# Kernel tuning notes

Hardware: AMD Instinct MI355X
Metric: run time of the kernel (lower is better)

Reference implementation:

```python
import jax, jax.numpy as jnp
import numpy as np

O, T = 2000, 6000
DIN, DW, DG, H = 2048, 300, 512, 512
VO, VR, L_EXTRA = 1000, 500, 4


def _mlp2(x, Wa, ba, Wb, bb):
    # two-layer MLP with ReLU after every Linear (sg2im build_mlp, final_nonlinearity=True)
    return jax.nn.relu(jax.nn.relu(x @ Wa + ba) @ Wb + bb)


def _triple_conv(obj_vecs, pred_vecs, s, o, Wa, ba, Wb, bb, W2a, b2a, W2b, b2b, alpha=1.0):
    # gather-by-edge -> edge MLP -> scatter-avg back to nodes (GraphTripleConv, pooling='avg')
    n_obj = obj_vecs.shape[0]
    dout = W2b.shape[1]
    cur = jnp.concatenate([obj_vecs[s], pred_vecs, obj_vecs[o]], axis=1)  # [T, 2*Din+Dp]
    t = _mlp2(cur, Wa, ba, Wb, bb)                                        # [T, 2H+Dout]
    new_s, new_p, new_o = t[:, :H], t[:, H:H + dout], t[:, H + dout:]
    pooled = jnp.zeros((n_obj, H), t.dtype).at[s].add(new_s).at[o].add(new_o)
    cnt = jnp.zeros((n_obj,), t.dtype).at[s].add(1.0).at[o].add(1.0)
    pooled = pooled / jnp.maximum(cnt, 1.0)[:, None]
    new_obj = alpha * _mlp2(pooled, W2a, b2a, W2b, b2b)
    return new_obj, new_p


def setup_inputs() -> dict:
    key = jax.random.key(0)
    ks = jax.random.split(key, 32)
    w = lambda k, sh: (jax.random.normal(k, sh, jnp.float32) * 0.02)
    inp = {
        'obj_embs': jax.random.normal(ks[0], (O, DIN), jnp.float32),
        'obj_nums': O,
        'pred_embs': jax.random.normal(ks[1], (T, DIN), jnp.float32),
        'pred_nums': T,
        'rels': jax.random.randint(ks[2], (T, 3), 0, VR, jnp.int64 if jax.config.read('jax_enable_x64') else jnp.int32),
        'objs': jax.random.randint(ks[3], (O,), 0, VO, jnp.int64 if jax.config.read('jax_enable_x64') else jnp.int32),
        # embedding tables
        'obj_table': jax.random.uniform(ks[4], (VO, DW), jnp.float32, -0.1, 0.1),
        'rel_table': jax.random.uniform(ks[5], (VR, DW), jnp.float32, -0.1, 0.1),
        # fusion layers: Linear(img_dim+word_dim -> img_dim) + relu
        'Wf_obj': w(ks[6], (DIN + DW, DIN)), 'bf_obj': jnp.zeros((DIN,), jnp.float32),
        'Wf_rel': w(ks[7], (DIN + DW, DIN)), 'bf_rel': jnp.zeros((DIN,), jnp.float32),
        # GraphTripleConv layer 1: net1 [3*DIN -> H -> 2H+DG], net2 [H -> H -> DG]
        'W1a': w(ks[8], (3 * DIN, H)), 'b1a': jnp.zeros((H,), jnp.float32),
        'W1b': w(ks[9], (H, 2 * H + DG)), 'b1b': jnp.zeros((2 * H + DG,), jnp.float32),
        'W2a': w(ks[10], (H, H)), 'b2a': jnp.zeros((H,), jnp.float32),
        'W2b': w(ks[11], (H, DG)), 'b2b': jnp.zeros((DG,), jnp.float32),
        # GraphTripleConvNet: 4 more layers, net1 [3*DG -> H -> 2H+DG], net2 [H -> H -> DG]
        'Ws1a': w(ks[12], (L_EXTRA, 3 * DG, H)), 'bs1a': jnp.zeros((L_EXTRA, H), jnp.float32),
        'Ws1b': w(ks[13], (L_EXTRA, H, 2 * H + DG)), 'bs1b': jnp.zeros((L_EXTRA, 2 * H + DG), jnp.float32),
        'Ws2a': w(ks[14], (L_EXTRA, H, H)), 'bs2a': jnp.zeros((L_EXTRA, H), jnp.float32),
        'Ws2b': w(ks[15], (L_EXTRA, H, DG)), 'bs2b': jnp.zeros((L_EXTRA, DG), jnp.float32),
    }
    return inp


def reference(obj_embs, obj_nums, pred_embs, pred_nums, rels, objs,
              obj_table, rel_table, Wf_obj, bf_obj, Wf_rel, bf_rel,
              W1a, b1a, W1b, b1b, W2a, b2a, W2b, b2b,
              Ws1a, bs1a, Ws1b, bs1b, Ws2a, bs2a, Ws2b, bs2b):
    s, p, o = rels[:, 0], rels[:, 1], rels[:, 2]
    # embedding lookup + concatenate-fusion (FusionLayer with relu)
    obj_vecs = jax.nn.relu(jnp.concatenate([obj_embs, obj_table[objs]], axis=1) @ Wf_obj + bf_obj)
    pred_vecs = jax.nn.relu(jnp.concatenate([pred_embs, rel_table[p]], axis=1) @ Wf_rel + bf_rel)
    # first GraphTripleConv (img_dim -> gconv_dim)
    obj_vecs, pred_vecs = _triple_conv(obj_vecs, pred_vecs, s, o,
                                       W1a, b1a, W1b, b1b, W2a, b2a, W2b, b2b)
    # GraphTripleConvNet: 4 more layers (gconv_dim -> gconv_dim)
    for i in range(L_EXTRA):
        obj_vecs, pred_vecs = _triple_conv(obj_vecs, pred_vecs, s, o,
                                           Ws1a[i], bs1a[i], Ws1b[i], bs1b[i],
                                           Ws2a[i], bs2a[i], Ws2b[i], bs2b[i])
    # no_imgnorm=True -> no final l2norm
    return obj_vecs, pred_vecs
```

## Files before the change

### kernel.cpp

```cpp
#include <hip/hip_runtime.h>

#define O_N 2000
#define T_N 6000
#define DIN 2048
#define DW  300
#define DG  512
#define HH_ 512

typedef __attribute__((ext_vector_type(8)))  short short8;
typedef __attribute__((ext_vector_type(16))) float f32x16;
typedef unsigned short u16;

__device__ __forceinline__ float4 ld4(const float* p) { return *(const float4*)p; }

__device__ __forceinline__ u16 rbf(float x) {
    unsigned int u = __float_as_uint(x);
    u += 0x7FFFu + ((u >> 16) & 1u);
    return (u16)(u >> 16);
}
__device__ __forceinline__ float fbf(u16 h) {
    return __uint_as_float((unsigned int)h << 16);
}
__device__ __forceinline__ void split3(float x, short& h, short& m, short& l) {
    u16 a = rbf(x);
    float r = x - fbf(a);
    u16 b = rbf(r);
    r -= fbf(b);
    u16 c = rbf(r);
    h = (short)a; m = (short)b; l = (short)c;
}

__device__ __forceinline__ void gl_lds16(u16* lds, const u16* g) {
    auto* gp = (const __attribute__((address_space(1))) unsigned int*)g;
    auto* lp = (__attribute__((address_space(3))) unsigned int*)lds;
    __builtin_amdgcn_global_load_lds(gp, lp, 16, 0, 0);
}

template<int BM, int BN, int KS>
__global__ __launch_bounds__(KS ? 512 : 256, KS ? 2 : (BM == 64 ? 4 : 2))
void gemm_mx(
    const u16* __restrict__ Ap, int MpA,
    const u16* __restrict__ Bp, int N, int KC, int M,
    const float* __restrict__ bias, int doRelu,
    float* __restrict__ C, int ldc,
    u16* __restrict__ Op, int MpO,
    const u16* __restrict__ Bp2, float* __restrict__ C2, u16* __restrict__ Op2,
    int nbx)
{
    static_assert(BM == 128 || BM == 64, "BM in {64,128}");
    constexpr int WM = BM / 2, WN = BN / 2;
    constexpr int FI = WM / 32, FJ = WN / 32;
    static_assert(!KS || FI == 2, "KS path needs FI=2");
    constexpr int UA = 6 * BM;
    constexpr int UB = 6 * BN;
    constexpr int NI = (UA + UB) / 64;
    constexpr int II = (NI + 3) / 4;
    constexpr int LDMIN = NI / 4;
    constexpr int BUF = (BM + BN) * 48;
    __shared__ u16 sm[(KS ? 6 : 3) * BUF];

    const int tid = threadIdx.x;
    const int w = tid >> 6, lane = tid & 63;
    const int wg = w & 3;
    const int g = KS ? (w >> 2) : 0;
    const int ln31 = lane & 31, lq = lane >> 5;

    int bx = blockIdx.x;
    const u16* Bpl = Bp; float* Cl = C; u16* Opl = Op;
    if (bx >= nbx) { bx -= nbx; Bpl = Bp2; Cl = C2; Opl = Op2; }
    const int n0 = bx * BN, m0 = blockIdx.y * BM;
    const long psA = (long)KC * MpA * 8;
    const long psB = (long)KC * N * 8;

    int c0 = 0, cn = KC;
    if (KS) { int h = (KC >> 2) << 1; c0 = g ? h : 0; cn = g ? (KC - h) : h; }
    const u16* ApG = Ap + (long)c0 * MpA * 8;
    const u16* BpG = Bpl + (long)c0 * N * 8;
    u16* smg = sm + g * 3 * BUF;

    const u16* gb[II]; int gstep[II]; int lob[II]; bool gv[II];
#pragma unroll
    for (int ii = 0; ii < II; ii++) {
        int n = wg + 4 * ii;
        gv[ii] = n < NI;
        int nn = gv[ii] ? n : 0;
        int u0 = nn * 64;
        bool isA = u0 < UA;
        int uu = isA ? u0 : u0 - UA;
        int dim = isA ? BM : BN;
        int row0 = uu % dim, pq = uu / dim;
        int q = pq & 1, p = pq >> 1;
        const u16* pb = (isA ? ApG : BpG) + (long)p * (isA ? psA : psB);
        int mp = isA ? MpA : N;
        gb[ii] = pb + ((long)q * mp + (isA ? m0 : n0) + row0 + lane) * 8;
        gstep[ii] = mp * 16;
        lob[ii] = (isA ? (pq * BM + row0) : (6 * BM + pq * BN + row0)) * 8;
    }

    f32x16 ah[FI][FJ], al[FI][FJ];
#pragma unroll
    for (int fi = 0; fi < FI; fi++)
#pragma unroll
        for (int fj = 0; fj < FJ; fj++)
#pragma unroll
            for (int r = 0; r < 16; r++) { ah[fi][fj][r] = 0.f; al[fi][fj][r] = 0.f; }

    const int T = cn >> 1;
#pragma unroll
    for (int ii = 0; ii < II; ii++)
        if (gv[ii]) gl_lds16(smg + lob[ii], gb[ii]);
    if (T > 1) {
#pragma unroll
        for (int ii = 0; ii < II; ii++)
            if (gv[ii]) gl_lds16(smg + BUF + lob[ii], gb[ii] + (long)gstep[ii]);
    }
#pragma unroll
    for (int ii = 0; ii < II; ii++) gb[ii] += (long)2 * gstep[ii];

    int cb = 0, sb = 2 * BUF;
    for (int t = 0; t < T; t++) {
        if (t + 1 < T) asm volatile("s_waitcnt vmcnt(%0)" :: "i"(LDMIN) : "memory");
        else           asm volatile("s_waitcnt vmcnt(0)" ::: "memory");
        __builtin_amdgcn_s_barrier();
        asm volatile("" ::: "memory");

        if (t + 2 < T) {
#pragma unroll
            for (int ii = 0; ii < II; ii++)
                if (gv[ii]) { gl_lds16(smg + sb + lob[ii], gb[ii]); gb[ii] += (long)gstep[ii]; }
        }

        const u16* ab = smg + cb;
        const u16* bb = ab + 6 * BM * 8;
        short8 af[FI][3], bf[FJ][3];
#pragma unroll
        for (int fi = 0; fi < FI; fi++)
#pragma unroll
            for (int p = 0; p < 3; p++)
                af[fi][p] = *(const short8*)(ab + ((p * 2 + lq) * BM + (wg >> 1) * WM + fi * 32 + ln31) * 8);
#pragma unroll
        for (int fj = 0; fj < FJ; fj++) {
            const int rB = (wg & 1) * WN + fj * 32 + ln31;
#pragma unroll
            for (int p = 0; p < 3; p++)
                bf[fj][p] = *(const short8*)(bb + ((p * 2 + lq) * BN + rB) * 8);
        }

#pragma unroll
        for (int fj = 0; fj < FJ; fj++) {
#pragma unroll
            for (int fi = 0; fi < FI; fi++) {
                ah[fi][fj] = __builtin_amdgcn_mfma_f32_32x32x16_bf16(af[fi][0], bf[fj][0], ah[fi][fj], 0, 0, 0);
                al[fi][fj] = __builtin_amdgcn_mfma_f32_32x32x16_bf16(af[fi][0], bf[fj][1], al[fi][fj], 0, 0, 0);
                al[fi][fj] = __builtin_amdgcn_mfma_f32_32x32x16_bf16(af[fi][1], bf[fj][0], al[fi][fj], 0, 0, 0);
                al[fi][fj] = __builtin_amdgcn_mfma_f32_32x32x16_bf16(af[fi][0], bf[fj][2], al[fi][fj], 0, 0, 0);
                al[fi][fj] = __builtin_amdgcn_mfma_f32_32x32x16_bf16(af[fi][1], bf[fj][1], al[fi][fj], 0, 0, 0);
                al[fi][fj] = __builtin_amdgcn_mfma_f32_32x32x16_bf16(af[fi][2], bf[fj][0], al[fi][fj], 0, 0, 0);
            }
        }

        cb += BUF; if (cb == 3 * BUF) cb = 0;
        sb += BUF; if (sb == 3 * BUF) sb = 0;
    }
    __syncthreads();

    float tv[FJ][16];
    if (KS) {
        constexpr int XW = FJ * 16 * 64;
        float* xs = (float*)sm;
        float* wrp = xs + (1 - g) * 4 * XW + wg * XW;
        if (g == 0) {
#pragma unroll
            for (int fj = 0; fj < FJ; fj++)
#pragma unroll
                for (int r = 0; r < 16; r++)
                    wrp[(fj * 16 + r) * 64 + lane] = ah[1][fj][r] + al[1][fj][r];
        } else {
#pragma unroll
            for (int fj = 0; fj < FJ; fj++)
#pragma unroll
                for (int r = 0; r < 16; r++)
                    wrp[(fj * 16 + r) * 64 + lane] = ah[0][fj][r] + al[0][fj][r];
        }
        __syncthreads();
        float* rdp = xs + g * 4 * XW + wg * XW;
        if (g == 0) {
#pragma unroll
            for (int fj = 0; fj < FJ; fj++)
#pragma unroll
                for (int r = 0; r < 16; r++)
                    tv[fj][r] = ah[0][fj][r] + al[0][fj][r] + rdp[(fj * 16 + r) * 64 + lane];
        } else {
#pragma unroll
            for (int fj = 0; fj < FJ; fj++)
#pragma unroll
                for (int r = 0; r < 16; r++)
                    tv[fj][r] = ah[1][fj][r] + al[1][fj][r] + rdp[(fj * 16 + r) * 64 + lane];
        }
        __syncthreads();
    }

    float* bounce = (float*)sm + w * 1184;
    const long psO = (long)N * MpO;
#pragma unroll
    for (int fi = 0; fi < FI; fi++) {
        if (KS && fi != g) continue;
#pragma unroll
        for (int fj = 0; fj < FJ; fj++) {
            const int colBase = n0 + (wg & 1) * WN + fj * 32;
            const int rowBase = m0 + (wg >> 1) * WM + fi * 32;
            float bv = bias ? bias[colBase + ln31] : 0.f;
            float v[16];
#pragma unroll
            for (int r = 0; r < 16; r++) {
                float s = KS ? tv[fj][r] : (ah[fi][fj][r] + al[fi][fj][r]);
                float x = s + bv;
                if (doRelu) x = fmaxf(x, 0.f);
                v[r] = x;
            }
            if (Cl) {
#pragma unroll
                for (int r = 0; r < 16; r++) {
                    int row = rowBase + (r & 3) + 8 * (r >> 2) + 4 * lq;
                    if (row < M)
                        Cl[(long)row * ldc + colBase + ln31] = v[r];
                }
            }
            if (Opl) {
#pragma unroll
                for (int r = 0; r < 16; r++)
                    bounce[((r & 3) + 8 * (r >> 2) + 4 * lq) * 36 + ln31] = v[r];
#pragma unroll
                for (int u = 0; u < 2; u++) {
                    int urow = ln31, uc = lq + 2 * u;
                    const float* rp = bounce + urow * 36 + uc * 8;
                    short8 h8, m8, l8;
#pragma unroll
                    for (int j = 0; j < 8; j++) {
                        short a, b, c2; split3(rp[j], a, b, c2);
                        h8[j] = a; m8[j] = b; l8[j] = c2;
                    }
                    long cIdx = (long)((colBase + uc * 8) >> 3);
                    long base = (cIdx * MpO + rowBase + urow) * 8;
                    *(short8*)(Opl + base) = h8;
                    *(short8*)(Opl + psO + base) = m8;
                    *(short8*)(Opl + 2 * psO + base) = l8;
                }
            }
        }
    }
}

__global__ __launch_bounds__(256) void split_b(
    const float* __restrict__ W, int K, int N, int KC,
    u16* __restrict__ Op)
{
    __shared__ float tl[64][65];
    const int tid = threadIdx.x;
    const int n0 = blockIdx.x * 64, k0 = blockIdx.y * 64;
    const long ps = (long)KC * N * 8;
#pragma unroll
    for (int l = 0; l < 4; l++) {
        int k = (tid >> 4) + l * 16;
        int nn = (tid & 15) << 2;
        float4 v = make_float4(0.f, 0.f, 0.f, 0.f);
        if (k0 + k < K) v = ld4(W + (long)(k0 + k) * N + n0 + nn);
        tl[k][nn] = v.x; tl[k][nn + 1] = v.y; tl[k][nn + 2] = v.z; tl[k][nn + 3] = v.w;
    }
    __syncthreads();
#pragma unroll
    for (int l = 0; l < 2; l++) {
        int u = tid + l * 256;
        int n = u & 63, c = u >> 6;
        short8 h8, m8, l8;
#pragma unroll
        for (int j = 0; j < 8; j++) {
            short a, b, c2; split3(tl[c * 8 + j][n], a, b, c2);
            h8[j] = a; m8[j] = b; l8[j] = c2;
        }
        long base = ((long)(k0 / 8 + c) * N + n0 + n) * 8;
        *(short8*)(Op + base) = h8;
        *(short8*)(Op + ps + base) = m8;
        *(short8*)(Op + 2 * ps + base) = l8;
    }
}

__device__ __forceinline__ void store_planes(u16* Op, long ps, long base, const float* x)
{
    short8 h8, m8, l8;
#pragma unroll
    for (int j = 0; j < 8; j++) {
        short a, b, c2; split3(x[j], a, b, c2);
        h8[j] = a; m8[j] = b; l8[j] = c2;
    }
    *(short8*)(Op + base) = h8;
    *(short8*)(Op + ps + base) = m8;
    *(short8*)(Op + 2 * ps + base) = l8;
}

__global__ __launch_bounds__(256) void split_concat_a(
    const float* __restrict__ E, int ldE, int KA,
    const float* __restrict__ Tab, int DWc,
    const int* __restrict__ idx, int idxStride,
    int mBase, int Mvalid, int Mp, int KC,
    u16* __restrict__ Op)
{
    int m = blockIdx.x * 256 + threadIdx.x;
    if (m >= Mp) return;
    int c = blockIdx.y;
    int gm = mBase + m;
    float x[8];
    if (gm >= Mvalid) {
#pragma unroll
        for (int j = 0; j < 8; j++) x[j] = 0.f;
    } else {
        int k0 = c * 8;
        if (k0 + 8 <= KA) {
            float4 a = ld4(E + (long)gm * ldE + k0);
            float4 b = ld4(E + (long)gm * ldE + k0 + 4);
            x[0] = a.x; x[1] = a.y; x[2] = a.z; x[3] = a.w;
            x[4] = b.x; x[5] = b.y; x[6] = b.z; x[7] = b.w;
        } else {
            const float* tr = Tab + (long)idx[(long)gm * idxStride] * DWc;
#pragma unroll
            for (int j = 0; j < 8; j++) {
                int k = k0 + j;
                x[j] = (k < KA) ? E[(long)gm * ldE + k]
                                : ((k - KA) < DWc ? tr[k - KA] : 0.f);
            }
        }
    }
    store_planes(Op, (long)KC * Mp * 8, ((long)c * Mp + m) * 8, x);
}

__global__ __launch_bounds__(256) void edge_planes(
    const float* __restrict__ PPv, const float* __restrict__ P1v,
    const float* __restrict__ P2v, const int* __restrict__ rels,
    const float* __restrict__ b1a, int Mp, u16* __restrict__ Op)
{
    int m = blockIdx.x * 256 + threadIdx.x;
    if (m >= Mp) return;
    int c = blockIdx.y;
    float x[8];
    if (m >= T_N) {
#pragma unroll
        for (int j = 0; j < 8; j++) x[j] = 0.f;
    } else {
        int s = rels[3 * m], o = rels[3 * m + 2];
        const float* pp = PPv + (long)m * HH_ + c * 8;
        const float* p1 = P1v + (long)s * HH_ + c * 8;
        const float* p2 = P2v + (long)o * HH_ + c * 8;
        const float* bb = b1a + c * 8;
#pragma unroll
        for (int j = 0; j < 8; j++)
            x[j] = fmaxf(pp[j] + p1[j] + p2[j] + bb[j], 0.f);
    }
    store_planes(Op, (long)64 * Mp * 8, ((long)c * Mp + m) * 8, x);
}

__global__ __launch_bounds__(256) void pool_planes(
    const float* __restrict__ PO, const int* __restrict__ CNT,
    int Mp, u16* __restrict__ Op)
{
    int m = blockIdx.x * 256 + threadIdx.x;
    if (m >= Mp) return;
    int c = blockIdx.y;
    float x[8];
    if (m >= O_N) {
#pragma unroll
        for (int j = 0; j < 8; j++) x[j] = 0.f;
    } else {
        int cc = CNT[m]; float cf = 1.f / (float)(cc < 1 ? 1 : cc);
#pragma unroll
        for (int j = 0; j < 8; j++) x[j] = PO[(long)m * HH_ + c * 8 + j] * cf;
    }
    store_planes(Op, (long)64 * Mp * 8, ((long)c * Mp + m) * 8, x);
}

__global__ __launch_bounds__(256) void predcopy_planes(
    const float* __restrict__ T2, int Mp, u16* __restrict__ Op)
{
    int m = blockIdx.x * 256 + threadIdx.x;
    if (m >= Mp) return;
    int c = blockIdx.y;
    float x[8];
    if (m >= T_N) {
#pragma unroll
        for (int j = 0; j < 8; j++) x[j] = 0.f;
    } else {
#pragma unroll
        for (int j = 0; j < 8; j++) x[j] = T2[(long)m * 1536 + 512 + c * 8 + j];
    }
    store_planes(Op, (long)64 * Mp * 8, ((long)c * Mp + m) * 8, x);
}

__global__ void predcopy_f32(const float* __restrict__ T2, float* __restrict__ dst)
{
    int i = blockIdx.x * 256 + threadIdx.x;
    if (i >= T_N * HH_ / 4) return;
    int e = i / (HH_ / 4);
    int j = (i % (HH_ / 4)) << 2;
    float4 v = ld4(T2 + (long)e * 1536 + 512 + j);
    *(float4*)(dst + (long)e * HH_ + j) = v;
}

__global__ void count_edges(const int* __restrict__ rels, int* __restrict__ CNT)
{
    int e = blockIdx.x * 256 + threadIdx.x;
    if (e >= T_N) return;
    atomicAdd(CNT + rels[3 * e + 0], 1);
    atomicAdd(CNT + rels[3 * e + 2], 1);
}

__global__ void scatter_pool(const float* __restrict__ T2,
                             const int* __restrict__ rels,
                             float* __restrict__ PO)
{
    int e = blockIdx.x;
    int t = threadIdx.x;
    int s = rels[e * 3 + 0];
    int o = rels[e * 3 + 2];
#pragma unroll
    for (int u = 0; u < 2; u++) {
        int j = t + u * 256;
        unsafeAtomicAdd(PO + (long)s * HH_ + j, T2[(long)e * 1536 + j]);
        unsafeAtomicAdd(PO + (long)o * HH_ + j, T2[(long)e * 1536 + 1024 + j]);
    }
}

template<int BM, int BN>
static inline void GX(hipStream_t st, const u16* Ap, int MpA,
                      const u16* Bp, int N, int KC, int M,
                      const float* bias, int relu_,
                      float* C, int ldc, u16* Op, int MpO,
                      const u16* Bp2, float* C2, u16* Op2)
{
    int nbx = N / BN;
    int pair = (Bp2 != nullptr) ? 2 : 1;
    dim3 g(nbx * pair, MpA / BM), b(256);
    gemm_mx<BM, BN, 0><<<g, b, 0, st>>>(Ap, MpA, Bp, N, KC, M, bias, relu_,
                                        C, ldc, Op, MpO, Bp2, C2, Op2, nbx);
}

template<int BM, int BN>
static inline void GK2(hipStream_t st, const u16* Ap, int MpA,
                       const u16* Bp, int N, int KC, int M,
                       const float* bias, int relu_,
                       float* C, int ldc, u16* Op, int MpO)
{
    dim3 g(N / BN, MpA / BM), b(512);
    gemm_mx<BM, BN, 1><<<g, b, 0, st>>>(Ap, MpA, Bp, N, KC, M, bias, relu_,
                                        C, ldc, Op, MpO,
                                        nullptr, nullptr, nullptr, N / BN);
}

static inline void SB(hipStream_t st, const float* W, int K, int N, int KC, u16* Op)
{
    dim3 g(N / 64, KC / 8), b(256);
    split_b<<<g, b, 0, st>>>(W, K, N, KC, Op);
}

extern "C" void kernel_launch(void* const* d_in, const int* in_sizes, int n_in,
                              void* d_out, int out_size, void* d_ws, size_t ws_size,
                              hipStream_t stream)
{
    const float* obj_embs  = (const float*)d_in[0];
    const float* pred_embs = (const float*)d_in[2];
    const int*   rels      = (const int*)d_in[4];
    const int*   objs      = (const int*)d_in[5];
    const float* obj_table = (const float*)d_in[6];
    const float* rel_table = (const float*)d_in[7];
    const float* Wf_obj = (const float*)d_in[8];
    const float* bf_obj = (const float*)d_in[9];
    const float* Wf_rel = (const float*)d_in[10];
    const float* bf_rel = (const float*)d_in[11];
    const float* W1a = (const float*)d_in[12];
    const float* b1a = (const float*)d_in[13];
    const float* W1b = (const float*)d_in[14];
    const float* b1b = (const float*)d_in[15];
    const float* W2a = (const float*)d_in[16];
    const float* b2a = (const float*)d_in[17];
    const float* W2b = (const float*)d_in[18];
    const float* b2b = (const float*)d_in[19];
    const float* Ws1a = (const float*)d_in[20];
    const float* bs1a = (const float*)d_in[21];
    const float* Ws1b = (const float*)d_in[22];
    const float* bs1b = (const float*)d_in[23];
    const float* Ws2a = (const float*)d_in[24];
    const float* bs2a = (const float*)d_in[25];
    const float* Ws2b = (const float*)d_in[26];
    const float* bs2b = (const float*)d_in[27];
    float* out = (float*)d_out;

    unsigned char* B8 = (unsigned char*)d_ws;
    constexpr size_t S1O  = 0;
    constexpr size_t S2O  = 29097984;
    constexpr size_t S3AO = 54263808;
    constexpr size_t ZSZ  = 86507520;
    constexpr size_t T2O  = 0;
    constexpr size_t TTO  = 36864000;
    constexpr size_t PVO  = 55345152;
    constexpr size_t PLO  = 73826304;
    constexpr size_t OVO  = 80117760;
    constexpr size_t S3BO = ZSZ;
    constexpr size_t S3CO = S3BO + 6291456;
    constexpr size_t PPO  = S3CO + 6291456;
    constexpr size_t P1O  = PPO + 12288000;
    constexpr size_t P2O  = P1O + 4096000;
    constexpr size_t CNO  = P2O + 4096000;

    u16* S1  = (u16*)(B8 + S1O);
    u16* S2  = (u16*)(B8 + S2O);
    u16* S3A = (u16*)(B8 + S3AO);
    u16* S3B = (u16*)(B8 + S3BO);
    u16* S3C = (u16*)(B8 + S3CO);
    float* T2 = (float*)(B8 + T2O);
    u16* TTp  = (u16*)(B8 + TTO);
    u16* Hp   = (u16*)(B8 + TTO);
    u16* PVp  = (u16*)(B8 + PVO);
    u16* PLp  = (u16*)(B8 + PLO);
    u16* OVp  = (u16*)(B8 + OVO);
    float* PP = (float*)(B8 + PPO);
    float* P1 = (float*)(B8 + P1O);
    float* P2 = (float*)(B8 + P2O);
    float* PO = P1;
    int* CNT  = (int*)(B8 + CNO);

    hipMemsetAsync(CNT, 0, O_N * sizeof(int), stream);
    hipLaunchKernelGGL(count_edges, dim3((T_N + 255) / 256), dim3(256), 0, stream, rels, CNT);

    SB(stream, Wf_obj, DIN + DW, DIN, 296, S3A);
    {
        dim3 g(8, 296), b(256);
        split_concat_a<<<g, b, 0, stream>>>(obj_embs, DIN, DIN, obj_table, DW,
                                            objs, 1, 0, O_N, 2048, 296, S1);
    }
    GK2<128, 128>(stream, S1, 2048, S3A, DIN, 296, O_N, bf_obj, 1,
                  nullptr, 0, S2, 2048);
    SB(stream, W1a, DIN, HH_, 256, S3B);
    SB(stream, W1a + (size_t)2 * DIN * HH_, DIN, HH_, 256, S3C);
    GX<64, 64>(stream, S2, 2048, S3B, HH_, 256, O_N, nullptr, 0,
               P1, HH_, nullptr, 0, S3C, P2, nullptr);
    SB(stream, Wf_rel, DIN + DW, DIN, 296, S3A);
    SB(stream, W1a + (size_t)DIN * HH_, DIN, HH_, 256, S3B);
    for (int ch = 0; ch < 3; ch++) {
        int ch0 = ch * 2048;
        int mp  = (ch == 2) ? 1920 : 2048;
        int mv  = (ch == 2) ? 1904 : 2048;
        dim3 g((mp + 255) / 256, 296), b(256);
        split_concat_a<<<g, b, 0, stream>>>(pred_embs, DIN, DIN, rel_table, DW,
                                            rels + 1, 3, ch0, T_N, mp, 296, S1);
        GK2<128, 128>(stream, S1, mp, S3A, DIN, 296, mv, bf_rel, 1,
                      nullptr, 0, S2, mp);
        GX<64, 64>(stream, S2, mp, S3B, HH_, 256, mv, nullptr, 0,
                   PP + (size_t)ch0 * HH_, HH_, nullptr, 0,
                   nullptr, nullptr, nullptr);
    }

    for (int L = 0; L < 5; L++) {
        const float* bb1a = (L == 0) ? b1a : (bs1a + (size_t)(L - 1) * HH_);
        const float* w1b  = (L == 0) ? W1b : (Ws1b + (size_t)(L - 1) * HH_ * 1536);
        const float* bb1b = (L == 0) ? b1b : (bs1b + (size_t)(L - 1) * 1536);
        const float* w2a  = (L == 0) ? W2a : (Ws2a + (size_t)(L - 1) * HH_ * HH_);
        const float* bb2a = (L == 0) ? b2a : (bs2a + (size_t)(L - 1) * HH_);
        const float* w2b  = (L == 0) ? W2b : (Ws2b + (size_t)(L - 1) * HH_ * DG);
        const float* bb2b = (L == 0) ? b2b : (bs2b + (size_t)(L - 1) * DG);

        if (L > 0) {
            const float* w1a = Ws1a + (size_t)(L - 1) * 3 * HH_ * HH_;
            SB(stream, w1a, HH_, HH_, 64, S3B);
            SB(stream, w1a + (size_t)2 * HH_ * HH_, HH_, HH_, 64, S3C);
            GX<64, 64>(stream, OVp, 2048, S3B, HH_, 64, O_N, nullptr, 0,
                       P1, HH_, nullptr, 0, S3C, P2, nullptr);
            SB(stream, w1a + (size_t)HH_ * HH_, HH_, HH_, 64, S3B);
            GX<64, 64>(stream, PVp, 6016, S3B, HH_, 64, T_N, nullptr, 0,
                       PP, HH_, nullptr, 0, nullptr, nullptr, nullptr);
        }

        {
            dim3 g(24, 64), b(256);
            edge_planes<<<g, b, 0, stream>>>(PP, P1, P2, rels, bb1a, 6016, TTp);
        }
        SB(stream, w1b, HH_, 1536, 64, S3C);
        GX<128, 128>(stream, TTp, 6016, S3C, 1536, 64, T_N, bb1b, 1,
                     T2, 1536, nullptr, 0, nullptr, nullptr, nullptr);
        hipMemsetAsync(PO, 0, (size_t)O_N * HH_ * sizeof(float), stream);
        hipLaunchKernelGGL(scatter_pool, dim3(T_N), dim3(256), 0, stream, T2, rels, PO);
        {
            dim3 g(8, 64), b(256);
            pool_planes<<<g, b, 0, stream>>>(PO, CNT, 2048, PLp);
        }
        SB(stream, w2a, HH_, HH_, 64, S3B);
        GX<64, 64>(stream, PLp, 2048, S3B, HH_, 64, O_N, bb2a, 1,
                   nullptr, 0, Hp, 2048, nullptr, nullptr, nullptr);
        SB(stream, w2b, HH_, DG, 64, S3C);
        if (L < 4) {
            GX<64, 64>(stream, Hp, 2048, S3C, DG, 64, O_N, bb2b, 1,
                       nullptr, 0, OVp, 2048, nullptr, nullptr, nullptr);
            dim3 g(24, 64), b(256);
            predcopy_planes<<<g, b, 0, stream>>>(T2, 6016, PVp);
        } else {
            GX<64, 64>(stream, Hp, 2048, S3C, DG, 64, O_N, bb2b, 1,
                       out, DG, nullptr, 0, nullptr, nullptr, nullptr);
            hipLaunchKernelGGL(predcopy_f32, dim3((T_N * HH_ / 4 + 255) / 256),
                               dim3(256), 0, stream, T2, out + (size_t)O_N * DG);
        }
    }
}
```

Before: 1.781 ms.

## Interleave LDS fragment loads with MFMA quadrants in split-K GEMM path

For the split-K (KS) GEMM variant, the main loop is restructured into four quadrant phases. Each phase loads the next A/B fragments from LDS and issues part of the global-to-LDS prefetch while the previous quadrant's MFMAs run. Barriers and s_setprio around each MFMA cluster keep the waves in step and favour matrix issue, and the next tile's first fragments are prefetched into registers. The non-KS path is unchanged. The cost is many more barriers per K step and extra register pressure from the double-buffered fragments.

```diff
diff --git a/kernel.cpp b/kernel.cpp
--- a/kernel.cpp
+++ b/kernel.cpp
@@ -35,6 +35,14 @@
     auto* lp = (__attribute__((address_space(3))) unsigned int*)lds;
     __builtin_amdgcn_global_load_lds(gp, lp, 16, 0, 0);
 }
+
+#define MFMA_Q(AX, BX, AH, AL) \
+    AH = __builtin_amdgcn_mfma_f32_32x32x16_bf16(AX[0], BX[0], AH, 0, 0, 0); \
+    AL = __builtin_amdgcn_mfma_f32_32x32x16_bf16(AX[0], BX[1], AL, 0, 0, 0); \
+    AL = __builtin_amdgcn_mfma_f32_32x32x16_bf16(AX[1], BX[0], AL, 0, 0, 0); \
+    AL = __builtin_amdgcn_mfma_f32_32x32x16_bf16(AX[0], BX[2], AL, 0, 0, 0); \
+    AL = __builtin_amdgcn_mfma_f32_32x32x16_bf16(AX[1], BX[1], AL, 0, 0, 0); \
+    AL = __builtin_amdgcn_mfma_f32_32x32x16_bf16(AX[2], BX[0], AL, 0, 0, 0);
 
 template<int BM, int BN, int KS>
 __global__ __launch_bounds__(KS ? 512 : 256, KS ? 2 : (BM == 64 ? 4 : 2))
@@ -50,7 +58,7 @@
     static_assert(BM == 128 || BM == 64, "BM in {64,128}");
     constexpr int WM = BM / 2, WN = BN / 2;
     constexpr int FI = WM / 32, FJ = WN / 32;
-    static_assert(!KS || FI == 2, "KS path needs FI=2");
+    static_assert(!KS || (FI == 2 && FJ == 2), "KS path needs 2x2 quadrants");
     constexpr int UA = 6 * BM;
     constexpr int UB = 6 * BN;
     constexpr int NI = (UA + UB) / 64;
@@ -106,61 +114,165 @@
             for (int r = 0; r < 16; r++) { ah[fi][fj][r] = 0.f; al[fi][fj][r] = 0.f; }
 
     const int T = cn >> 1;
-#pragma unroll
-    for (int ii = 0; ii < II; ii++)
-        if (gv[ii]) gl_lds16(smg + lob[ii], gb[ii]);
-    if (T > 1) {
+
+    if constexpr (KS) {
+#pragma unroll
+        for (int ii = 0; ii < II; ii++)
+            if (gv[ii]) gl_lds16(smg + lob[ii], gb[ii]);
 #pragma unroll
         for (int ii = 0; ii < II; ii++)
             if (gv[ii]) gl_lds16(smg + BUF + lob[ii], gb[ii] + (long)gstep[ii]);
-    }
-#pragma unroll
-    for (int ii = 0; ii < II; ii++) gb[ii] += (long)2 * gstep[ii];
-
-    int cb = 0, sb = 2 * BUF;
-    for (int t = 0; t < T; t++) {
-        if (t + 1 < T) asm volatile("s_waitcnt vmcnt(%0)" :: "i"(LDMIN) : "memory");
-        else           asm volatile("s_waitcnt vmcnt(0)" ::: "memory");
+#pragma unroll
+        for (int ii = 0; ii < II; ii++) gb[ii] += (long)2 * gstep[ii];
+
+        asm volatile("s_waitcnt vmcnt(%0)" :: "i"(II) : "memory");
         __builtin_amdgcn_s_barrier();
-        asm volatile("" ::: "memory");
-
-        if (t + 2 < T) {
+
+        const int rA = (wg >> 1) * WM + ln31;
+        const int rB = (wg & 1) * WN + ln31;
+        short8 A0[3], A1[3], B0[3], B1[3], A0n[3], B0n[3];
+        {
+            const u16* ab = smg;
+            const u16* bb = ab + 6 * BM * 8;
+#pragma unroll
+            for (int p = 0; p < 3; p++) {
+                A0[p] = *(const short8*)(ab + ((p * 2 + lq) * BM + rA) * 8);
+                B0[p] = *(const short8*)(bb + ((p * 2 + lq) * BN + rB) * 8);
+            }
+        }
+
+        int cb = 0, nb = BUF, sb = 2 * BUF;
+        for (int t = 0; t < T; t++) {
+            const u16* ab  = smg + cb;
+            const u16* bb  = ab + 6 * BM * 8;
+            const u16* abn = smg + nb;
+            const u16* bbn = abn + 6 * BM * 8;
+            const bool stg = (t + 2) < T;
+            const bool nxt = (t + 1) < T;
+
+#pragma unroll
+            for (int p = 0; p < 3; p++)
+                A1[p] = *(const short8*)(ab + ((p * 2 + lq) * BM + rA + 32) * 8);
+            if (stg) {
+#pragma unroll
+                for (int ii = 0; ii < 3; ii++)
+                    if (gv[ii]) gl_lds16(smg + sb + lob[ii], gb[ii]);
+            }
+            __builtin_amdgcn_s_barrier();
+            asm volatile("s_waitcnt lgkmcnt(0)" ::: "memory");
+            __builtin_amdgcn_s_setprio(1);
+            MFMA_Q(A0, B0, ah[0][0], al[0][0]);
+            __builtin_amdgcn_s_setprio(0);
+            __builtin_amdgcn_s_barrier();
+
+#pragma unroll
+            for (int p = 0; p < 3; p++)
+                B1[p] = *(const short8*)(bb + ((p * 2 + lq) * BN + rB + 32) * 8);
+            if (stg) {
+#pragma unroll
+                for (int ii = 3; ii < II; ii++)
+                    if (gv[ii]) gl_lds16(smg + sb + lob[ii], gb[ii]);
+            }
+            __builtin_amdgcn_s_barrier();
+            asm volatile("s_waitcnt lgkmcnt(0)" ::: "memory");
+            __builtin_amdgcn_s_setprio(1);
+            MFMA_Q(A1, B0, ah[1][0], al[1][0]);
+            __builtin_amdgcn_s_setprio(0);
+            __builtin_amdgcn_s_barrier();
+
+            if (nxt) {
+                if (stg) asm volatile("s_waitcnt vmcnt(%0)" :: "i"(II) : "memory");
+                else     asm volatile("s_waitcnt vmcnt(0)" ::: "memory");
+#pragma unroll
+                for (int p = 0; p < 3; p++)
+                    A0n[p] = *(const short8*)(abn + ((p * 2 + lq) * BM + rA) * 8);
+            }
+            __builtin_amdgcn_s_barrier();
+            asm volatile("s_waitcnt lgkmcnt(0)" ::: "memory");
+            __builtin_amdgcn_s_setprio(1);
+            MFMA_Q(A0, B1, ah[0][1], al[0][1]);
+            __builtin_amdgcn_s_setprio(0);
+            __builtin_amdgcn_s_barrier();
+
+            if (nxt) {
+#pragma unroll
+                for (int p = 0; p < 3; p++)
+                    B0n[p] = *(const short8*)(bbn + ((p * 2 + lq) * BN + rB) * 8);
+            }
+            __builtin_amdgcn_s_barrier();
+            asm volatile("s_waitcnt lgkmcnt(0)" ::: "memory");
+            __builtin_amdgcn_s_setprio(1);
+            MFMA_Q(A1, B1, ah[1][1], al[1][1]);
+            __builtin_amdgcn_s_setprio(0);
+            __builtin_amdgcn_s_barrier();
+
+            if (nxt) {
+#pragma unroll
+                for (int p = 0; p < 3; p++) { A0[p] = A0n[p]; B0[p] = B0n[p]; }
+            }
+            if (stg) {
+#pragma unroll
+                for (int ii = 0; ii < II; ii++) gb[ii] += (long)gstep[ii];
+            }
+            int tmp = cb; cb = nb; nb = sb; sb = tmp;
+        }
+    } else {
+#pragma unroll
+        for (int ii = 0; ii < II; ii++)
+            if (gv[ii]) gl_lds16(smg + lob[ii], gb[ii]);
+        if (T > 1) {
 #pragma unroll
             for (int ii = 0; ii < II; ii++)
-                if (gv[ii]) { gl_lds16(smg + sb + lob[ii], gb[ii]); gb[ii] += (long)gstep[ii]; }
-        }
-
-        const u16* ab = smg + cb;
-        const u16* bb = ab + 6 * BM * 8;
-        short8 af[FI][3], bf[FJ][3];
-#pragma unroll
-        for (int fi = 0; fi < FI; fi++)
-#pragma unroll
-            for (int p = 0; p < 3; p++)
-                af[fi][p] = *(const short8*)(ab + ((p * 2 + lq) * BM + (wg >> 1) * WM + fi * 32 + ln31) * 8);
-#pragma unroll
-        for (int fj = 0; fj < FJ; fj++) {
-            const int rB = (wg & 1) * WN + fj * 32 + ln31;
-#pragma unroll
-            for (int p = 0; p < 3; p++)
-                bf[fj][p] = *(const short8*)(bb + ((p * 2 + lq) * BN + rB) * 8);
-        }
-
-#pragma unroll
-        for (int fj = 0; fj < FJ; fj++) {
-#pragma unroll
-            for (int fi = 0; fi < FI; fi++) {
-                ah[fi][fj] = __builtin_amdgcn_mfma_f32_32x32x16_bf16(af[fi][0], bf[fj][0], ah[fi][fj], 0, 0, 0);
-                al[fi][fj] = __builtin_amdgcn_mfma_f32_32x32x16_bf16(af[fi][0], bf[fj][1], al[fi][fj], 0, 0, 0);
-                al[fi][fj] = __builtin_amdgcn_mfma_f32_32x32x16_bf16(af[fi][1], bf[fj][0], al[fi][fj], 0, 0, 0);
-                al[fi][fj] = __builtin_amdgcn_mfma_f32_32x32x16_bf16(af[fi][0], bf[fj][2], al[fi][fj], 0, 0, 0);
-                al[fi][fj] = __builtin_amdgcn_mfma_f32_32x32x16_bf16(af[fi][1], bf[fj][1], al[fi][fj], 0, 0, 0);
-                al[fi][fj] = __builtin_amdgcn_mfma_f32_32x32x16_bf16(af[fi][2], bf[fj][0], al[fi][fj], 0, 0, 0);
-            }
-        }
-
-        cb += BUF; if (cb == 3 * BUF) cb = 0;
-        sb += BUF; if (sb == 3 * BUF) sb = 0;
+                if (gv[ii]) gl_lds16(smg + BUF + lob[ii], gb[ii] + (long)gstep[ii]);
+        }
+#pragma unroll
+        for (int ii = 0; ii < II; ii++) gb[ii] += (long)2 * gstep[ii];
+
+        int cb = 0, sb = 2 * BUF;
+        for (int t = 0; t < T; t++) {
+            if (t + 1 < T) asm volatile("s_waitcnt vmcnt(%0)" :: "i"(LDMIN) : "memory");
+            else           asm volatile("s_waitcnt vmcnt(0)" ::: "memory");
+            __builtin_amdgcn_s_barrier();
+            asm volatile("" ::: "memory");
+
+            if (t + 2 < T) {
+#pragma unroll
+                for (int ii = 0; ii < II; ii++)
+                    if (gv[ii]) { gl_lds16(smg + sb + lob[ii], gb[ii]); gb[ii] += (long)gstep[ii]; }
+            }
+
+            const u16* ab = smg + cb;
+            const u16* bb = ab + 6 * BM * 8;
+            short8 af[FI][3], bf[FJ][3];
+#pragma unroll
+            for (int fi = 0; fi < FI; fi++)
+#pragma unroll
+                for (int p = 0; p < 3; p++)
+                    af[fi][p] = *(const short8*)(ab + ((p * 2 + lq) * BM + (wg >> 1) * WM + fi * 32 + ln31) * 8);
+#pragma unroll
+            for (int fj = 0; fj < FJ; fj++) {
+                const int rB = (wg & 1) * WN + fj * 32 + ln31;
+#pragma unroll
+                for (int p = 0; p < 3; p++)
+                    bf[fj][p] = *(const short8*)(bb + ((p * 2 + lq) * BN + rB) * 8);
+            }
+
+#pragma unroll
+            for (int fj = 0; fj < FJ; fj++) {
+#pragma unroll
+                for (int fi = 0; fi < FI; fi++) {
+                    ah[fi][fj] = __builtin_amdgcn_mfma_f32_32x32x16_bf16(af[fi][0], bf[fj][0], ah[fi][fj], 0, 0, 0);
+                    al[fi][fj] = __builtin_amdgcn_mfma_f32_32x32x16_bf16(af[fi][0], bf[fj][1], al[fi][fj], 0, 0, 0);
+                    al[fi][fj] = __builtin_amdgcn_mfma_f32_32x32x16_bf16(af[fi][1], bf[fj][0], al[fi][fj], 0, 0, 0);
+                    al[fi][fj] = __builtin_amdgcn_mfma_f32_32x32x16_bf16(af[fi][0], bf[fj][2], al[fi][fj], 0, 0, 0);
+                    al[fi][fj] = __builtin_amdgcn_mfma_f32_32x32x16_bf16(af[fi][1], bf[fj][1], al[fi][fj], 0, 0, 0);
+                    al[fi][fj] = __builtin_amdgcn_mfma_f32_32x32x16_bf16(af[fi][2], bf[fj][0], al[fi][fj], 0, 0, 0);
+                }
+            }
+
+            cb += BUF; if (cb == 3 * BUF) cb = 0;
+            sb += BUF; if (sb == 3 * BUF) sb = 0;
+        }
     }
     __syncthreads();
 
```

Result: no change. 1.796 ms (+0.8%).
